# Kernel tuning notes

Hardware: AMD Instinct MI355X
Metric: run time of the kernel (lower is better)

Reference implementation:

```python
import jax, jax.numpy as jnp
import numpy as np

N_NODES = 50000


def gcn_conv(x, src, dst, W, b, n_nodes):
    """PyG GCNConv: add self-loops, symmetric D^-1/2 (A+I) D^-1/2 normalization,
    linear transform, scatter-add aggregation, bias."""
    loop = jnp.arange(n_nodes, dtype=src.dtype)
    s = jnp.concatenate([src, loop])
    d = jnp.concatenate([dst, loop])
    deg = jax.ops.segment_sum(jnp.ones_like(s, dtype=x.dtype), d, num_segments=n_nodes)
    dinv = jnp.where(deg > 0, jax.lax.rsqrt(deg), 0.0)
    norm = dinv[s] * dinv[d]                      # [E+N]
    h = x @ W                                     # [N, out] dense GEMM first (PyG order)
    msg = h[s] * norm[:, None]                    # gather + scale: [E+N, out]
    out = jax.ops.segment_sum(msg, d, num_segments=n_nodes)  # scatter-add
    return out + b


def setup_inputs() -> dict:
    key = jax.random.key(0)
    k = jax.random.split(key, 4)
    N, E, IN, HID, OUT = N_NODES, 625000, 128, 128, 64
    return {
        "x": jax.random.normal(k[0], (N, IN), jnp.float32),
        "edge_index": jax.random.randint(k[1], (2, E), 0, N, dtype=jnp.int32),
        "W1": jax.random.normal(k[2], (IN, HID), jnp.float32) / np.float32(np.sqrt(IN)),
        "b1": jnp.zeros((HID,), jnp.float32),
        "W2": jax.random.normal(k[3], (HID, OUT), jnp.float32) / np.float32(np.sqrt(HID)),
        "b2": jnp.zeros((OUT,), jnp.float32),
    }


def reference(x, edge_index, W1, b1, W2, b2):
    src, dst = edge_index[0], edge_index[1]
    # n_layers = 2: conv1 + ReLU, then final conv without activation
    h = jax.nn.relu(gcn_conv(x, src, dst, W1, b1, N_NODES))
    return gcn_conv(h, src, dst, W2, b2, N_NODES)
```

## Files before the change

kernel.cpp:

```cpp
#include <hip/hip_runtime.h>
#include <math.h>


#define RPB 32
#define CAP 8192
#define PA_BLK 256

typedef _Float16 h8  __attribute__((ext_vector_type(8)));
typedef _Float16 h2t __attribute__((ext_vector_type(2)));
typedef float    f4v __attribute__((ext_vector_type(4)));

__device__ __forceinline__ unsigned pkh(float a, float b) {
    auto r = __builtin_amdgcn_cvt_pkrtz(a, b);
    return __builtin_bit_cast(unsigned, r);
}
__device__ __forceinline__ void accw(float* g, float c, unsigned w) {
    h2t p = __builtin_bit_cast(h2t, w);
    g[0] += c * (float)p.x;
    g[1] += c * (float)p.y;
}
__device__ __forceinline__ void acc16h(float* ga, float c, uint4 u0, uint4 u1) {
    accw(ga + 0, c, u0.x); accw(ga + 2, c, u0.y);
    accw(ga + 4, c, u0.z); accw(ga + 6, c, u0.w);
    accw(ga + 8, c, u1.x); accw(ga + 10, c, u1.y);
    accw(ga + 12, c, u1.z); accw(ga + 14, c, u1.w);
}
__device__ __forceinline__ void acc8h(float* ga, float c, uint4 u) {
    accw(ga + 0, c, u.x); accw(ga + 2, c, u.y);
    accw(ga + 4, c, u.z); accw(ga + 6, c, u.w);
}

__global__ __launch_bounds__(256) void k_prep(const int* __restrict__ src,
                                              const int* __restrict__ dst, int e,
                                              int* __restrict__ bcur,
                                              unsigned* __restrict__ ebuf, int EPB,
                                              const float* __restrict__ W1,
                                              const float* __restrict__ W2,
                                              unsigned short* __restrict__ Wpk1,
                                              unsigned short* __restrict__ Wpk2) {
    const int blk = (int)blockIdx.x;
    if (blk < PA_BLK) {
        __shared__ int h[256];
        __shared__ int gb[256];
        const int t = threadIdx.x;
        h[t] = 0;
        __syncthreads();
        const int e0 = blk * EPB;
        const int e1 = min(e0 + EPB, e);
        for (int i = e0 + t; i < e1; i += 256)
            atomicAdd(&h[((unsigned)dst[i]) >> 8], 1);
        __syncthreads();
        const int c = h[t];
        if (c > 0) gb[t] = atomicAdd(&bcur[t], c);
        h[t] = 0;
        __syncthreads();
        for (int i = e0 + t; i < e1; i += 256) {
            const unsigned d  = (unsigned)dst[i];
            const int bk = d >> 8;
            const int p  = atomicAdd(&h[bk], 1) + gb[bk];
            if (p < CAP) ebuf[((size_t)bk << 13) + p] = ((d & 255u) << 24) | (unsigned)src[i];
        }
    } else if (blk < PA_BLK + 8) {
        int idx = (blk - PA_BLK) * 256 + threadIdx.x;
        int l = idx & 63, g = idx >> 6;
        int kt = g >> 3, nt = g & 7;
        const float* Wp = W1 + (size_t)(kt * 32 + ((l >> 4) << 3)) * 128 + nt * 16 + (l & 15);
        uint4 o;
        o.x = pkh(Wp[0],   Wp[128]);
        o.y = pkh(Wp[256], Wp[384]);
        o.z = pkh(Wp[512], Wp[640]);
        o.w = pkh(Wp[768], Wp[896]);
        *(uint4*)&Wpk1[(size_t)idx * 8] = o;
    } else {
        int idx = (blk - PA_BLK - 8) * 256 + threadIdx.x;
        if (idx < 1024) {
            int l = idx & 63, g = idx >> 6;
            int kt = g >> 2, nt = g & 3;
            const float* Wp = W2 + (size_t)(kt * 32 + ((l >> 4) << 3)) * 64 + nt * 16 + (l & 15);
            uint4 o;
            o.x = pkh(Wp[0],   Wp[64]);
            o.y = pkh(Wp[128], Wp[192]);
            o.z = pkh(Wp[256], Wp[320]);
            o.w = pkh(Wp[384], Wp[448]);
            *(uint4*)&Wpk2[(size_t)idx * 8] = o;
        }
    }
}

__global__ __launch_bounds__(256) void k_bucket(const unsigned* __restrict__ ebuf,
                                                const int* __restrict__ bcur,
                                                int* __restrict__ rowptr,
                                                float* __restrict__ dinv,
                                                unsigned* __restrict__ erec,
                                                int n, int nbk, int e) {
    __shared__ int sc[256];
    __shared__ int h[256];
    __shared__ int loc[256];
    __shared__ int sBase;
    const int t = threadIdx.x;
    const int b = blockIdx.x;

    const int v = (t < nbk) ? min(bcur[t], CAP) : 0;
    sc[t] = v;
    __syncthreads();
    for (int off = 1; off < 256; off <<= 1) {
        int u = (t >= off) ? sc[t - off] : 0;
        __syncthreads();
        sc[t] += u;
        __syncthreads();
    }
    if (t == b) sBase = sc[t] - v;
    if (b == 0 && t == 0) rowptr[n] = e;
    h[t] = 0;
    __syncthreads();

    const int cb = min(bcur[b], CAP);
    const unsigned* __restrict__ eb = ebuf + ((size_t)b << 13);
    for (int i = t; i < cb; i += 256) atomicAdd(&h[eb[i] >> 24], 1);
    __syncthreads();
    const int deg = h[t];
    sc[t] = deg;
    __syncthreads();
    for (int off = 1; off < 256; off <<= 1) {
        int u = (t >= off) ? sc[t - off] : 0;
        __syncthreads();
        sc[t] += u;
        __syncthreads();
    }
    loc[t] = sc[t] - deg;
    const int id = (b << 8) + t;
    if (id < n) {
        rowptr[id] = sBase + loc[t];
        dinv[id]   = rsqrtf((float)(deg + 1));
    }
    h[t] = 0;
    __syncthreads();
    unsigned* __restrict__ outp = erec + sBase;
    for (int i = t; i < cb; i += 256) {
        const unsigned r  = eb[i];
        const int      lb = r >> 24;
        const int      p  = atomicAdd(&h[lb], 1);
        outp[loc[lb] + p] = r & 0xFFFFFFu;
    }
}

__global__ __launch_bounds__(256) void k_scale(const float* __restrict__ x,
                                               const float* __restrict__ dinv,
                                               unsigned short* __restrict__ xs,
                                               unsigned short* __restrict__ h2s,
                                               int n) {
    const int gid = blockIdx.x * 256 + threadIdx.x;
    const int i8  = gid * 8;
    const int row = i8 >> 7;
    if (row < n) {
        const float wd = dinv[row];
        float4 v0 = *(const float4*)&x[i8];
        float4 v1 = *(const float4*)&x[i8 + 4];
        uint4 o;
        o.x = pkh(v0.x * wd, v0.y * wd); o.y = pkh(v0.z * wd, v0.w * wd);
        o.z = pkh(v1.x * wd, v1.y * wd); o.w = pkh(v1.z * wd, v1.w * wd);
        *(uint4*)&xs[i8] = o;
    } else if (row == n) {
        *(uint4*)&xs[i8] = make_uint4(0, 0, 0, 0);
        const int k = gid - n * 16;
        if (k < 8) *(uint4*)&h2s[(size_t)n * 64 + k * 8] = make_uint4(0, 0, 0, 0);
    }
}

__global__ __launch_bounds__(256, 4) void fused_l1(const unsigned short* __restrict__ Xs,
                                                   const unsigned short* __restrict__ Wpk1,
                                                   const float* __restrict__ bias1,
                                                   const unsigned short* __restrict__ Wpk2,
                                                   const int* __restrict__ rowptr,
                                                   const unsigned* __restrict__ erec,
                                                   const float* __restrict__ dinv,
                                                   unsigned short* __restrict__ h2s,
                                                   int n) {
    __shared__ __align__(16) char sMb[RPB * 256];

    const int t    = threadIdx.x;
    const int row0 = blockIdx.x * RPB;

    {
        const int r = t >> 3;
        const int b = t & 7;
        const int d = row0 + r;
        float ga[16] = {};
        if (d < n) {
            const float wd = dinv[d];
            const uint4* P = (const uint4*)(Xs + ((size_t)d << 7)) + b * 2;
            acc16h(ga, wd, P[0], P[1]);
            const int beg = rowptr[d], end = rowptr[d + 1];
            int j = beg;
            const unsigned Z = (unsigned)n;
            unsigned s0 = (j     < end) ? erec[j]     : Z;
            unsigned s1 = (j + 1 < end) ? erec[j + 1] : Z;
            unsigned s2 = (j + 2 < end) ? erec[j + 2] : Z;
            unsigned s3 = (j + 3 < end) ? erec[j + 3] : Z;
            while (j < end) {
                const unsigned c0 = s0, c1 = s1, c2 = s2, c3 = s3;
                const int jn = j + 4;
                s0 = (jn     < end) ? erec[jn]     : Z;
                s1 = (jn + 1 < end) ? erec[jn + 1] : Z;
                s2 = (jn + 2 < end) ? erec[jn + 2] : Z;
                s3 = (jn + 3 < end) ? erec[jn + 3] : Z;
                const uint4* P0 = (const uint4*)(Xs + ((size_t)c0 << 7)) + b * 2;
                const uint4* P1 = (const uint4*)(Xs + ((size_t)c1 << 7)) + b * 2;
                const uint4* P2 = (const uint4*)(Xs + ((size_t)c2 << 7)) + b * 2;
                const uint4* P3 = (const uint4*)(Xs + ((size_t)c3 << 7)) + b * 2;
                uint4 a0 = P0[0], a1 = P0[1];
                uint4 b0 = P1[0], b1 = P1[1];
                uint4 d0 = P2[0], d1 = P2[1];
                uint4 e0 = P3[0], e1 = P3[1];
                acc16h(ga, wd, a0, a1);
                acc16h(ga, wd, b0, b1);
                acc16h(ga, wd, d0, d1);
                acc16h(ga, wd, e0, e1);
                j = jn;
            }
        }
        uint4 o0, o1;
        o0.x = pkh(ga[0],  ga[1]);  o0.y = pkh(ga[2],  ga[3]);
        o0.z = pkh(ga[4],  ga[5]);  o0.w = pkh(ga[6],  ga[7]);
        o1.x = pkh(ga[8],  ga[9]);  o1.y = pkh(ga[10], ga[11]);
        o1.z = pkh(ga[12], ga[13]); o1.w = pkh(ga[14], ga[15]);
        const int swz = (r & 7) << 4;
        *(uint4*)(sMb + ((r * 256 + b * 32)      ^ swz)) = o0;
        *(uint4*)(sMb + ((r * 256 + b * 32 + 16) ^ swz)) = o1;
    }
    __syncthreads();

    const int w  = t >> 6;
    const int l  = t & 63;
    const int lr = l & 15;
    const int lk = (l >> 4) << 4;
    const int sz = (lr & 7) << 4;

    f4v acc[2][2] = {};
#pragma unroll
    for (int kt = 0; kt < 4; ++kt) {
        const int kb = kt * 64 + lk;
        h8 a0 = *(const h8*)(sMb + ((lr * 256 + kb)        ^ sz));
        h8 a1 = *(const h8*)(sMb + (((lr + 16) * 256 + kb) ^ sz));
        const h8* Bp = (const h8*)Wpk1 + (kt * 8 + w * 2) * 64 + l;
        h8 b0 = Bp[0];
        h8 b1 = Bp[64];
        acc[0][0] = __builtin_amdgcn_mfma_f32_16x16x32_f16(a0, b0, acc[0][0], 0, 0, 0);
        acc[0][1] = __builtin_amdgcn_mfma_f32_16x16x32_f16(a0, b1, acc[0][1], 0, 0, 0);
        acc[1][0] = __builtin_amdgcn_mfma_f32_16x16x32_f16(a1, b0, acc[1][0], 0, 0, 0);
        acc[1][1] = __builtin_amdgcn_mfma_f32_16x16x32_f16(a1, b1, acc[1][1], 0, 0, 0);
    }
    __syncthreads();

    {
        const float bb0 = bias1[w * 32 + lr];
        const float bb1 = bias1[w * 32 + 16 + lr];
        const int c0 = (w * 32 + lr) * 2;
        const int c1 = (w * 32 + 16 + lr) * 2;
#pragma unroll
        for (int mt = 0; mt < 2; ++mt)
#pragma unroll
            for (int v = 0; v < 4; ++v) {
                const int row = mt * 16 + ((l >> 4) << 2) + v;
                const int rs  = (row & 7) << 4;
                float o0 = fmaxf(acc[mt][0][v] + bb0, 0.f);
                float o1 = fmaxf(acc[mt][1][v] + bb1, 0.f);
                *(_Float16*)(sMb + ((row * 256 + c0) ^ rs)) = (_Float16)o0;
                *(_Float16*)(sMb + ((row * 256 + c1) ^ rs)) = (_Float16)o1;
            }
    }
    __syncthreads();

    f4v acc2[2] = {};
#pragma unroll
    for (int kt = 0; kt < 4; ++kt) {
        const int kb = kt * 64 + lk;
        h8 a0 = *(const h8*)(sMb + ((lr * 256 + kb)        ^ sz));
        h8 a1 = *(const h8*)(sMb + (((lr + 16) * 256 + kb) ^ sz));
        h8 b  = *((const h8*)Wpk2 + (kt * 4 + w) * 64 + l);
        acc2[0] = __builtin_amdgcn_mfma_f32_16x16x32_f16(a0, b, acc2[0], 0, 0, 0);
        acc2[1] = __builtin_amdgcn_mfma_f32_16x16x32_f16(a1, b, acc2[1], 0, 0, 0);
    }
#pragma unroll
    for (int mt = 0; mt < 2; ++mt)
#pragma unroll
        for (int v = 0; v < 4; ++v) {
            const int row = row0 + mt * 16 + ((l >> 4) << 2) + v;
            if (row < n) {
                _Float16 hv = (_Float16)(acc2[mt][v] * dinv[row]);
                h2s[(size_t)row * 64 + w * 16 + lr] = __builtin_bit_cast(unsigned short, hv);
            }
        }
}

__global__ __launch_bounds__(256, 6) void k_out(const unsigned short* __restrict__ h2s,
                                                const float* __restrict__ b2,
                                                const int* __restrict__ rowptr,
                                                const unsigned* __restrict__ erec,
                                                const float* __restrict__ dinv,
                                                float* __restrict__ out, int n) {
    const int t = threadIdx.x;
    const int r = t >> 3;
    const int b = t & 7;
    const int d = blockIdx.x * RPB + r;
    if (d >= n) return;

    const float wd = dinv[d];
    float ga[8] = {};
    {
        uint4 u = *((const uint4*)(h2s + ((size_t)d << 6)) + b);
        acc8h(ga, wd, u);
    }
    const int beg = rowptr[d], end = rowptr[d + 1];
    int j = beg;
    const unsigned Z = (unsigned)n;
    unsigned s0 = (j     < end) ? erec[j]     : Z;
    unsigned s1 = (j + 1 < end) ? erec[j + 1] : Z;
    unsigned s2 = (j + 2 < end) ? erec[j + 2] : Z;
    unsigned s3 = (j + 3 < end) ? erec[j + 3] : Z;
    while (j < end) {
        const unsigned c0 = s0, c1 = s1, c2 = s2, c3 = s3;
        const int jn = j + 4;
        s0 = (jn     < end) ? erec[jn]     : Z;
        s1 = (jn + 1 < end) ? erec[jn + 1] : Z;
        s2 = (jn + 2 < end) ? erec[jn + 2] : Z;
        s3 = (jn + 3 < end) ? erec[jn + 3] : Z;
        uint4 u0 = *((const uint4*)(h2s + ((size_t)c0 << 6)) + b);
        uint4 u1 = *((const uint4*)(h2s + ((size_t)c1 << 6)) + b);
        uint4 u2 = *((const uint4*)(h2s + ((size_t)c2 << 6)) + b);
        uint4 u3 = *((const uint4*)(h2s + ((size_t)c3 << 6)) + b);
        acc8h(ga, wd, u0);
        acc8h(ga, wd, u1);
        acc8h(ga, wd, u2);
        acc8h(ga, wd, u3);
        j = jn;
    }
    const float4 bv0 = *(const float4*)&b2[b * 8];
    const float4 bv1 = *(const float4*)&b2[b * 8 + 4];
    float* O = out + (size_t)d * 64 + b * 8;
    *(float4*)O       = make_float4(ga[0] + bv0.x, ga[1] + bv0.y, ga[2] + bv0.z, ga[3] + bv0.w);
    *(float4*)(O + 4) = make_float4(ga[4] + bv1.x, ga[5] + bv1.y, ga[6] + bv1.z, ga[7] + bv1.w);
}


extern "C" void kernel_launch(void* const* d_in, const int* in_sizes, int n_in,
                              void* d_out, int out_size, void* d_ws, size_t ws_size,
                              hipStream_t stream) {
    const float* x  = (const float*)d_in[0];
    const int*   ei = (const int*)d_in[1];
    const float* W1 = (const float*)d_in[2];
    const float* b1 = (const float*)d_in[3];
    const float* W2 = (const float*)d_in[4];
    const float* b2 = (const float*)d_in[5];
    float* out = (float*)d_out;

    const int N = in_sizes[0] / 128;
    const int E = in_sizes[1] / 2;
    const int* src = ei;
    const int* dst = ei + E;
    const int NBK = (N + 255) >> 8;
    if (NBK > 256) return;

    size_t off = 0;
    char* base = (char*)d_ws;
    auto carve = [&](size_t bytes) -> void* {
        void* p = base + off;
        off += (bytes + 255) & ~(size_t)255;
        return p;
    };
    int*      bcur   = (int*)carve(256 * 4);
    int*      rowptr = (int*)carve((size_t)(N + 1) * 4);
    float*    dinv   = (float*)carve((size_t)N * 4);
    unsigned* erec   = (unsigned*)carve((size_t)E * 4);
    unsigned* ebuf   = (unsigned*)carve((size_t)256 * CAP * 4);
    unsigned short* xs   = (unsigned short*)carve((size_t)(N + 1) * 128 * 2);
    unsigned short* h2s  = (unsigned short*)carve((size_t)(N + 1) * 64 * 2);
    unsigned short* Wpk1 = (unsigned short*)carve(128 * 128 * 2);
    unsigned short* Wpk2 = (unsigned short*)carve(128 * 64 * 2);

    if (off > ws_size) return;

    const int EPB = (E + PA_BLK - 1) / PA_BLK;
    hipMemsetAsync(bcur, 0, 256 * 4, stream);
    k_prep<<<PA_BLK + 12, 256, 0, stream>>>(src, dst, E, bcur, ebuf, EPB,
                                            W1, W2, Wpk1, Wpk2);
    k_bucket<<<NBK, 256, 0, stream>>>(ebuf, bcur, rowptr, dinv, erec, N, NBK, E);
    k_scale<<<((N + 1) * 16 + 255) / 256, 256, 0, stream>>>(x, dinv, xs, h2s, N);

    const int nblk = (N + RPB - 1) / RPB;
    fused_l1<<<nblk, 256, 0, stream>>>(xs, Wpk1, b1, Wpk2, rowptr, erec, dinv, h2s, N);
    k_out<<<nblk, 256, 0, stream>>>(h2s, b2, rowptr, erec, dinv, out, N);
}
```

Measured before the change: 150.0 us.

## Fuse feature scaling into bucket kernel and deepen gather unroll to eight

Moves the dinv-scaled fp16 conversion of x into the CSR bucket kernel, using per-block dinv kept in shared memory, and removes the separate k_scale launch. The gather loops in both aggregation kernels now issue eight neighbour loads per iteration instead of four to raise memory-level parallelism. fused_l1 also switches each thread's two 16-byte row loads from adjacent chunks to chunks half a row apart, with a matching shared-memory layout. Costs are more registers from the deeper unroll, which may reduce occupancy, and a bucket kernel with only about 196 blocks doing the scaling work.

```diff
diff --git a/kernel.cpp b/kernel.cpp
--- a/kernel.cpp
+++ b/kernel.cpp
@@ -18,12 +18,6 @@
     h2t p = __builtin_bit_cast(h2t, w);
     g[0] += c * (float)p.x;
     g[1] += c * (float)p.y;
-}
-__device__ __forceinline__ void acc16h(float* ga, float c, uint4 u0, uint4 u1) {
-    accw(ga + 0, c, u0.x); accw(ga + 2, c, u0.y);
-    accw(ga + 4, c, u0.z); accw(ga + 6, c, u0.w);
-    accw(ga + 8, c, u1.x); accw(ga + 10, c, u1.y);
-    accw(ga + 12, c, u1.z); accw(ga + 14, c, u1.w);
 }
 __device__ __forceinline__ void acc8h(float* ga, float c, uint4 u) {
     accw(ga + 0, c, u.x); accw(ga + 2, c, u.y);
@@ -92,10 +86,14 @@
                                                 int* __restrict__ rowptr,
                                                 float* __restrict__ dinv,
                                                 unsigned* __restrict__ erec,
+                                                const float* __restrict__ x,
+                                                unsigned short* __restrict__ xs,
+                                                unsigned short* __restrict__ h2s,
                                                 int n, int nbk, int e) {
     __shared__ int sc[256];
     __shared__ int h[256];
     __shared__ int loc[256];
+    __shared__ float sdinv[256];
     __shared__ int sBase;
     const int t = threadIdx.x;
     const int b = blockIdx.x;
@@ -129,10 +127,13 @@
     }
     loc[t] = sc[t] - deg;
     const int id = (b << 8) + t;
+    float wdl = 0.f;
     if (id < n) {
+        wdl = rsqrtf((float)(deg + 1));
         rowptr[id] = sBase + loc[t];
-        dinv[id]   = rsqrtf((float)(deg + 1));
-    }
+        dinv[id]   = wdl;
+    }
+    sdinv[t] = wdl;
     h[t] = 0;
     __syncthreads();
     unsigned* __restrict__ outp = erec + sBase;
@@ -142,28 +143,26 @@
         const int      p  = atomicAdd(&h[lb], 1);
         outp[loc[lb] + p] = r & 0xFFFFFFu;
     }
-}
-
-__global__ __launch_bounds__(256) void k_scale(const float* __restrict__ x,
-                                               const float* __restrict__ dinv,
-                                               unsigned short* __restrict__ xs,
-                                               unsigned short* __restrict__ h2s,
-                                               int n) {
-    const int gid = blockIdx.x * 256 + threadIdx.x;
-    const int i8  = gid * 8;
-    const int row = i8 >> 7;
-    if (row < n) {
-        const float wd = dinv[row];
-        float4 v0 = *(const float4*)&x[i8];
-        float4 v1 = *(const float4*)&x[i8 + 4];
-        uint4 o;
-        o.x = pkh(v0.x * wd, v0.y * wd); o.y = pkh(v0.z * wd, v0.w * wd);
-        o.z = pkh(v1.x * wd, v1.y * wd); o.w = pkh(v1.z * wd, v1.w * wd);
-        *(uint4*)&xs[i8] = o;
-    } else if (row == n) {
-        *(uint4*)&xs[i8] = make_uint4(0, 0, 0, 0);
-        const int k = gid - n * 16;
-        if (k < 8) *(uint4*)&h2s[(size_t)n * 64 + k * 8] = make_uint4(0, 0, 0, 0);
+
+    const int rbase = b << 8;
+    const int nrow  = min(256, n - rbase);
+#pragma unroll
+    for (int k = 0; k < 16; ++k) {
+        const int rr = (t >> 4) + k * 16;
+        if (rr < nrow) {
+            const float w = sdinv[rr];
+            const size_t base8 = ((size_t)(rbase + rr)) * 128 + (t & 15) * 8;
+            float4 v0 = *(const float4*)&x[base8];
+            float4 v1 = *(const float4*)&x[base8 + 4];
+            uint4 o;
+            o.x = pkh(v0.x * w, v0.y * w); o.y = pkh(v0.z * w, v0.w * w);
+            o.z = pkh(v1.x * w, v1.y * w); o.w = pkh(v1.z * w, v1.w * w);
+            *(uint4*)&xs[base8] = o;
+        }
+    }
+    if (b == 0) {
+        if (t < 16)      *(uint4*)&xs [(size_t)n * 128 + t * 8]        = make_uint4(0, 0, 0, 0);
+        else if (t < 24) *(uint4*)&h2s[(size_t)n * 64  + (t - 16) * 8] = make_uint4(0, 0, 0, 0);
     }
 }
 
@@ -188,35 +187,41 @@
         float ga[16] = {};
         if (d < n) {
             const float wd = dinv[d];
-            const uint4* P = (const uint4*)(Xs + ((size_t)d << 7)) + b * 2;
-            acc16h(ga, wd, P[0], P[1]);
+            {
+                const uint4* P = (const uint4*)(Xs + ((size_t)d << 7));
+                uint4 sa = P[b];
+                uint4 sb = P[8 + b];
+                acc8h(ga, wd, sa);
+                acc8h(ga + 8, wd, sb);
+            }
             const int beg = rowptr[d], end = rowptr[d + 1];
             int j = beg;
             const unsigned Z = (unsigned)n;
-            unsigned s0 = (j     < end) ? erec[j]     : Z;
-            unsigned s1 = (j + 1 < end) ? erec[j + 1] : Z;
-            unsigned s2 = (j + 2 < end) ? erec[j + 2] : Z;
-            unsigned s3 = (j + 3 < end) ? erec[j + 3] : Z;
-            while (j < end) {
-                const unsigned c0 = s0, c1 = s1, c2 = s2, c3 = s3;
-                const int jn = j + 4;
-                s0 = (jn     < end) ? erec[jn]     : Z;
-                s1 = (jn + 1 < end) ? erec[jn + 1] : Z;
-                s2 = (jn + 2 < end) ? erec[jn + 2] : Z;
-                s3 = (jn + 3 < end) ? erec[jn + 3] : Z;
-                const uint4* P0 = (const uint4*)(Xs + ((size_t)c0 << 7)) + b * 2;
-                const uint4* P1 = (const uint4*)(Xs + ((size_t)c1 << 7)) + b * 2;
-                const uint4* P2 = (const uint4*)(Xs + ((size_t)c2 << 7)) + b * 2;
-                const uint4* P3 = (const uint4*)(Xs + ((size_t)c3 << 7)) + b * 2;
-                uint4 a0 = P0[0], a1 = P0[1];
-                uint4 b0 = P1[0], b1 = P1[1];
-                uint4 d0 = P2[0], d1 = P2[1];
-                uint4 e0 = P3[0], e1 = P3[1];
-                acc16h(ga, wd, a0, a1);
-                acc16h(ga, wd, b0, b1);
-                acc16h(ga, wd, d0, d1);
-                acc16h(ga, wd, e0, e1);
-                j = jn;
+            if (j < end) {
+                unsigned s[8];
+#pragma unroll
+                for (int q = 0; q < 8; ++q) s[q] = (j + q < end) ? erec[j + q] : Z;
+                while (j < end) {
+                    const int jn = j + 8;
+                    uint4 rA[8], rB[8];
+#pragma unroll
+                    for (int q = 0; q < 8; ++q) {
+                        const uint4* Pq = (const uint4*)(Xs + ((size_t)s[q] << 7));
+                        rA[q] = Pq[b];
+                        rB[q] = Pq[8 + b];
+                    }
+                    unsigned sn[8];
+#pragma unroll
+                    for (int q = 0; q < 8; ++q) sn[q] = (jn + q < end) ? erec[jn + q] : Z;
+#pragma unroll
+                    for (int q = 0; q < 8; ++q) {
+                        acc8h(ga, wd, rA[q]);
+                        acc8h(ga + 8, wd, rB[q]);
+                    }
+#pragma unroll
+                    for (int q = 0; q < 8; ++q) s[q] = sn[q];
+                    j = jn;
+                }
             }
         }
         uint4 o0, o1;
@@ -225,8 +230,8 @@
         o1.x = pkh(ga[8],  ga[9]);  o1.y = pkh(ga[10], ga[11]);
         o1.z = pkh(ga[12], ga[13]); o1.w = pkh(ga[14], ga[15]);
         const int swz = (r & 7) << 4;
-        *(uint4*)(sMb + ((r * 256 + b * 32)      ^ swz)) = o0;
-        *(uint4*)(sMb + ((r * 256 + b * 32 + 16) ^ swz)) = o1;
+        *(uint4*)(sMb + ((r * 256 + b * 16)       ^ swz)) = o0;
+        *(uint4*)(sMb + ((r * 256 + 128 + b * 16) ^ swz)) = o1;
     }
     __syncthreads();
 
@@ -314,26 +319,25 @@
     const int beg = rowptr[d], end = rowptr[d + 1];
     int j = beg;
     const unsigned Z = (unsigned)n;
-    unsigned s0 = (j     < end) ? erec[j]     : Z;
-    unsigned s1 = (j + 1 < end) ? erec[j + 1] : Z;
-    unsigned s2 = (j + 2 < end) ? erec[j + 2] : Z;
-    unsigned s3 = (j + 3 < end) ? erec[j + 3] : Z;
-    while (j < end) {
-        const unsigned c0 = s0, c1 = s1, c2 = s2, c3 = s3;
-        const int jn = j + 4;
-        s0 = (jn     < end) ? erec[jn]     : Z;
-        s1 = (jn + 1 < end) ? erec[jn + 1] : Z;
-        s2 = (jn + 2 < end) ? erec[jn + 2] : Z;
-        s3 = (jn + 3 < end) ? erec[jn + 3] : Z;
-        uint4 u0 = *((const uint4*)(h2s + ((size_t)c0 << 6)) + b);
-        uint4 u1 = *((const uint4*)(h2s + ((size_t)c1 << 6)) + b);
-        uint4 u2 = *((const uint4*)(h2s + ((size_t)c2 << 6)) + b);
-        uint4 u3 = *((const uint4*)(h2s + ((size_t)c3 << 6)) + b);
-        acc8h(ga, wd, u0);
-        acc8h(ga, wd, u1);
-        acc8h(ga, wd, u2);
-        acc8h(ga, wd, u3);
-        j = jn;
+    if (j < end) {
+        unsigned s[8];
+#pragma unroll
+        for (int q = 0; q < 8; ++q) s[q] = (j + q < end) ? erec[j + q] : Z;
+        while (j < end) {
+            const int jn = j + 8;
+            uint4 u[8];
+#pragma unroll
+            for (int q = 0; q < 8; ++q)
+                u[q] = *((const uint4*)(h2s + ((size_t)s[q] << 6)) + b);
+            unsigned sn[8];
+#pragma unroll
+            for (int q = 0; q < 8; ++q) sn[q] = (jn + q < end) ? erec[jn + q] : Z;
+#pragma unroll
+            for (int q = 0; q < 8; ++q) acc8h(ga, wd, u[q]);
+#pragma unroll
+            for (int q = 0; q < 8; ++q) s[q] = sn[q];
+            j = jn;
+        }
     }
     const float4 bv0 = *(const float4*)&b2[b * 8];
     const float4 bv1 = *(const float4*)&b2[b * 8 + 4];
@@ -384,8 +388,8 @@
     hipMemsetAsync(bcur, 0, 256 * 4, stream);
     k_prep<<<PA_BLK + 12, 256, 0, stream>>>(src, dst, E, bcur, ebuf, EPB,
                                             W1, W2, Wpk1, Wpk2);
-    k_bucket<<<NBK, 256, 0, stream>>>(ebuf, bcur, rowptr, dinv, erec, N, NBK, E);
-    k_scale<<<((N + 1) * 16 + 255) / 256, 256, 0, stream>>>(x, dinv, xs, h2s, N);
+    k_bucket<<<NBK, 256, 0, stream>>>(ebuf, bcur, rowptr, dinv, erec,
+                                      x, xs, h2s, N, NBK, E);
 
     const int nblk = (N + RPB - 1) / RPB;
     fused_l1<<<nblk, 256, 0, stream>>>(xs, Wpk1, b1, Wpk2, rowptr, erec, dinv, h2s, N);
```

Result: slower. 245.4 us (+63.6%).
